# Kernel optimization log

Measured on AMD Instinct MI355X. Metric: run time of the kernel, lower is better.

Reference implementation:

```python
import jax, jax.numpy as jnp
import numpy as np

# ParamsJR('JR') defaults, all variances 0 -> fixed constants; w_bb and lm are the fit params.
DT = 1e-4                      # step_size
VMAX, V0, R = 5.0, 6.0, 0.56   # sigmoid params
U_UB = 500.0                   # u_2ndsys_ub
G_EFF = 0.01 + 1000.0          # lb + relu(g)
C1_EFF, C2_EFF = 0.01 + 135.0, 0.01 + 135.0 * 0.8
C3_EFF, C4_EFF = 0.01 + 135.0 * 0.25, 0.01 + 135.0 * 0.25
STD_EFF = 150.0 + 100.0        # noise_std_lb + relu(std_in)
K_EFF = 0.5 + 5.0              # k_lb + relu(k)
A_EFF, a_EFF = 3.25, 1.0 + 100.0   # 0+relu(A), 1+relu(a)
B_EFF, b_EFF = 22.0, 1.0 + 50.0    # 0+relu(B), 1+relu(b)
CY0, Y0, MU = 5.0, 2.0, 0.5
CONDUCT_LB = 1.5


def _sig(x):
    return VMAX / (1.0 + jnp.exp(R * (V0 - x)))


def _sys2nd(A, a, u, x, v):
    return A * a * u - 2.0 * a * v - a * a * x


def _sat(x):  # state saturation 1000*tanh(x/1000)
    return 1000.0 * jnp.tanh(x / 1000.0)


def setup_inputs() -> dict:
    N, H, B, OUT, BUF = 200, 20, 400, 64, 500
    key = jax.random.key(0)
    ks = jax.random.split(key, 7)
    return {
        "input": jax.random.normal(ks[0], (N, H, B), jnp.float32),
        "noise_in": jax.random.normal(ks[1], (N, H, B, 3), jnp.float32),
        "noise_out": jax.random.normal(ks[2], (N, B), jnp.float32),
        "hx": jax.random.uniform(ks[3], (N, 6), jnp.float32),
        "hE": jnp.zeros((N, BUF), jnp.float32),
        "w_bb": jnp.full((N, N), 0.05, jnp.float32),  # zeros + 0.05 init
        "lm": jax.random.normal(ks[4], (OUT, N), jnp.float32),
        "sc": jax.random.uniform(ks[5], (N, N), jnp.float32),
        "dist": jax.random.randint(ks[6], (N, N), 0, 100, dtype=jnp.int32),
    }


def _forward(input, noise_in, noise_out, hx, hE, w_bb, lm, sc, delays):
    OUT = lm.shape[0]
    # connectivity normalization (done once, outside the time loop, as in torch)
    w = jnp.exp(w_bb) * sc
    wl = jnp.log1p(0.5 * (w + w.T))
    w_n = wl / jnp.linalg.norm(wl)             # (N,N)
    dg = -jnp.diag(jnp.sum(w_n, axis=1))       # (N,N) Laplacian diagonal
    # lead-field normalization: rowwise L1 (torch: sqrt(lm**2).sum(1)), then column mean-center
    lm1 = lm / jnp.abs(lm).sum(axis=1, keepdims=True)
    lm_t = lm1 - lm1.sum(axis=0, keepdims=True) / OUT

    def inner(carry, xs):
        M, E, I, Mv, Ev, Iv, hEb = carry
        u, nE = xs                                              # (N,1) each
        Ed = jnp.take_along_axis(hEb, delays, axis=1)           # delayed M buffer
        LEd = jnp.sum(w_n * Ed.T, axis=1, keepdims=True)        # (N,1)
        rM = _sig(E - I)
        rE = STD_EFF * nE + G_EFF * (LEd + dg @ E) + C2_EFF * _sig(C1_EFF * M)
        rI = C4_EFF * _sig(C3_EFF * M)
        ddM = M + DT * Mv
        ddE = E + DT * Ev
        ddI = I + DT * Iv
        ddMv = Mv + DT * _sys2nd(A_EFF, a_EFF, U_UB * jnp.tanh(rM / U_UB), M, Mv)
        ddEv = Ev + DT * _sys2nd(A_EFF, a_EFF, K_EFF * u + U_UB * jnp.tanh(rE / U_UB), E, Ev)
        ddIv = Iv + DT * _sys2nd(B_EFF, b_EFF, U_UB * jnp.tanh(rI / U_UB), I, Iv)
        M, E, I = _sat(ddM), _sat(ddE), _sat(ddI)
        Mv, Ev, Iv = _sat(ddMv), _sat(ddEv), _sat(ddIv)
        hEb = hEb.at[:, 0].set(M[:, 0])
        return (M, E, I, Mv, Ev, Iv, hEb), None

    def outer(carry, xs):
        u_tr, n_tr = xs                                         # (H,N,1) each
        carry, _ = jax.lax.scan(inner, carry, (u_tr, n_tr))
        M, E, I, Mv, Ev, Iv, hEb = carry
        hEb = jnp.concatenate([M, hEb[:, :-1]], axis=1)         # shift delay buffer per TR
        eeg = CY0 * (lm_t @ (E - I)) - Y0                       # (OUT,1)
        return (M, E, I, Mv, Ev, Iv, hEb), eeg[:, 0]

    M, E, I = hx[:, 0:1], hx[:, 1:2], hx[:, 2:3]
    Mv, Ev, Iv = hx[:, 3:4], hx[:, 4:5], hx[:, 5:6]
    u_all = jnp.transpose(input, (2, 1, 0))[..., None]          # (B,H,N,1)
    nE_all = jnp.transpose(noise_in[..., 0], (2, 1, 0))[..., None]
    carry, eeg = jax.lax.scan(outer, (M, E, I, Mv, Ev, Iv, hE), (u_all, nE_all))
    M, E, I, Mv, Ev, Iv, _ = carry
    current_state = jnp.concatenate([M, E, I, Mv, Ev, Iv], axis=1)  # (N,6)
    return eeg.T, current_state                                 # eeg_batch (OUT,B)


def reference(input, noise_in, noise_out, hx, hE, w_bb, lm, sc, dist):
    delays = (dist.astype(jnp.float32) / (CONDUCT_LB + MU)).astype(jnp.int32)
    return _forward(input, noise_in, noise_out, hx, hE, w_bb, lm, sc, delays)
```

## Files before the change

kernel.cpp:

```cpp
#include <hip/hip_runtime.h>
#include <math.h>

namespace {

constexpr int N_   = 200;
constexpr int H_   = 20;
constexpr int B_   = 400;
constexpr int OUT_ = 64;
constexpr int BUF_ = 500;
constexpr int NT_  = 1024;
constexpr int HD_  = 50;
constexpr int HS_  = 51;
constexpr int GT0  = 224;
constexpr int NG_  = 800;
constexpr int EPT  = 50;
constexpr int CAP  = 16;
constexpr int UNR  = 12;

constexpr float L2E = 1.4426950408889634f;
constexpr float LN2 = 0.6931471805599453f;

constexpr float DT_  = 0.0001f;
constexpr float G_   = 1000.01f;
constexpr float C1_  = 135.01f;
constexpr float C2_  = 108.01f;
constexpr float C3_  = 33.76f;
constexpr float C4_  = 33.76f;
constexpr float STD_ = 250.0f;
constexpr float K_   = 5.5f;
constexpr float CY0_ = 5.0f;
constexpr float Y0_  = 2.0f;

constexpr float RL2E = 0.56f * L2E;
constexpr float V0R  = 6.0f * RL2E;
constexpr float TU_  = 2.0f * L2E / 500.0f;
constexpr float TS_  = 2.0f * L2E / 1000.0f;

constexpr float KMv = 0.9798f, KMu = 0.0328250f, KMx = 1.0201f;
constexpr float KEv = 0.9798f, KEu = 0.0328250f, KEx = 1.0201f;
constexpr float KIv = 0.9898f, KIu = 0.1122000f, KIx = 0.2601f;

__device__ __forceinline__ float fexp2(float x){ return __builtin_amdgcn_exp2f(x); }
__device__ __forceinline__ float flog2(float x){ return __builtin_amdgcn_logf(x); }
__device__ __forceinline__ float frcp (float x){ return __builtin_amdgcn_rcpf(x); }

__device__ __forceinline__ float sigf(float x){
    return 5.0f * frcp(1.0f + fexp2(fmaf(-RL2E, x, V0R)));
}
__device__ __forceinline__ float tanh500(float x){
    return 500.0f - 1000.0f * frcp(1.0f + fexp2(x * TU_));
}
__device__ __forceinline__ float satf(float x){
    return 1000.0f - 2000.0f * frcp(1.0f + fexp2(x * TS_));
}
__device__ __forceinline__ float wl_f(const float* __restrict__ wbb,
                                      const float* __restrict__ sc,
                                      int i, int j){
    float w0 = fexp2(wbb[i*N_+j]*L2E) * sc[i*N_+j];
    float w1 = fexp2(wbb[j*N_+i]*L2E) * sc[j*N_+i];
    return flog2(1.0f + 0.5f*(w0+w1)) * LN2;
}

__global__ void __launch_bounds__(NT_)
jansen_kernel(
    const float* __restrict__ input,
    const float* __restrict__ noise_in,
    const float* __restrict__ hx,
    const float* __restrict__ hEin,
    const float* __restrict__ wbb,
    const float* __restrict__ lm,
    const float* __restrict__ sc,
    const int*   __restrict__ dist,
    float* __restrict__ out,
    float2* __restrict__ tab)
{
    __shared__ float histT[N_*HS_];
    __shared__ float uslab[H_*N_];
    __shared__ float neslab[H_*N_];
    __shared__ float d0w_l[CAP*N_];
    __shared__ unsigned char d0j_l[CAP*N_];
    __shared__ float d1w_l[CAP*N_];
    __shared__ unsigned char d1j_l[CAP*N_];
    __shared__ float led_part[4*N_];
    __shared__ float mcol[2*N_];
    __shared__ float emi[N_];
    __shared__ float colmean[N_];
    __shared__ float lmrs[OUT_];
    __shared__ float red_s[NT_/64];
    __shared__ float norm_s;

    const int t = threadIdx.x;
    const bool isr = (t < N_);
    const bool isg = (t >= GT0);
    const int  gt  = t - GT0;
    const int  grow  = gt >> 2;
    const int  gslot = gt & 3;
    const int  jbase = gslot * EPT;
    const int  tb    = gt * EPT;

    int sidx[5];
    int goff[5];

    if (t < OUT_){
        float s2 = 0.f;
        for (int j=0;j<N_;++j) s2 += fabsf(lm[t*N_+j]);
        lmrs[t] = s2;
    }
    float M=0,E=0,I=0,Mv=0,Ev=0,Iv=0, rowsum=0, ledst=0;
    int cnt0=0, cnt1=0;
    #pragma unroll
    for (int r=0;r<5;++r){ sidx[r]=0; goff[r]=0; }
    if (isg){
        #pragma unroll
        for (int r=0;r<5;++r){
            int p = r*NG_ + gt;
            int hh = p / N_, ii = p - hh*N_;
            sidx[r] = hh*N_ + ii;
            goff[r] = ii*(H_*B_) + hh*B_;
            uslab[sidx[r]]  = input[goff[r]];
            neslab[sidx[r]] = noise_in[goff[r]*3];
        }
    }
    if (isr){
        for (int k=1;k<HD_;++k) histT[t*HS_ + (HD_-k)] = hEin[t*BUF_+k];
        mcol[t] = hEin[t*BUF_];
        M=hx[t*6+0]; E=hx[t*6+1]; I=hx[t*6+2];
        Mv=hx[t*6+3]; Ev=hx[t*6+4]; Iv=hx[t*6+5];
    }
    __syncthreads();

    float ss = 0.f, rs = 0.f;
    for (int m=0;m<EPT;++m){
        float w = 0.f; int d = 2;
        int j = jbase + m;
        if (isg){
            d = dist[j*N_+grow] >> 1;
            w = wl_f(wbb, sc, grow, j);
        }
        ss = fmaf(w,w,ss); rs += w;
        if (isg){
            int dm = (d<2) ? 2 : d;
            float ws = (d>=2) ? w : 0.f;
            tab[tb+m] = make_float2(ws, __uint_as_float((unsigned)j | ((unsigned)dm<<16)));
        }
    }
    if (isr){
        float cm=0.f;
        for (int o=0;o<OUT_;++o) cm += lm[o*N_+t] * frcp(lmrs[o]);
        colmean[t] = cm * (1.0f/(float)OUT_);
    }
    #pragma unroll
    for (int o=32;o>0;o>>=1) ss += __shfl_down(ss,o,64);
    if ((t&63)==0) red_s[t>>6] = ss;
    __syncthreads();
    if (t==0){ float tot=0.f; for (int w=0;w<NT_/64;++w) tot+=red_s[w]; norm_s = sqrtf(tot); }
    __syncthreads();
    const float inv = 1.0f / norm_s;
    if (isg){
        float* tf = (float*)tab;
        for (int m=0;m<EPT;++m) tf[2*(tb+m)] *= inv;
    }
    if (isg) led_part[gslot*N_+grow] = rs;

    float dw[UNR]; unsigned jpk[3];
    #pragma unroll
    for (int k=0;k<UNR;++k) dw[k] = 0.f;
    jpk[0]=jpk[1]=jpk[2]=0u;
    if (isr){
        #pragma unroll
        for (int k=0;k<UNR;++k){ d0w_l[k*N_+t]=0.f; d0j_l[k*N_+t]=0;
                                 d1w_l[k*N_+t]=0.f; d1j_l[k*N_+t]=0; }
        for (int j=0;j<N_;++j){
            int dd = dist[j*N_+t] >> 1;
            if (dd < 2){
                float w = wl_f(wbb, sc, t, j) * inv;
                if (dd==0){ if (cnt0<CAP){ d0w_l[cnt0*N_+t]=w; d0j_l[cnt0*N_+t]=(unsigned char)j; ++cnt0; } }
                else      { if (cnt1<CAP){ d1w_l[cnt1*N_+t]=w; d1j_l[cnt1*N_+t]=(unsigned char)j; ++cnt1; } }
            }
        }
        #pragma unroll
        for (int k=0;k<UNR;++k){
            dw[k] = d0w_l[k*N_+t];
            unsigned jv = d0j_l[k*N_+t];
            jpk[k>>2] |= jv << ((k&3)*8);
        }
    }
    __syncthreads();

    if (isr){
        rowsum = (led_part[t]+led_part[N_+t]+led_part[2*N_+t]+led_part[3*N_+t]) * inv;
    }
    __syncthreads();

    if (isg){
        float a0 = 0.f;
        for (int m=0;m<EPT;++m){
            float2 e = tab[tb+m];
            unsigned um = __float_as_uint(e.y);
            int c = HD_ - (int)(um>>16);
            a0 = fmaf(e.x, histT[(um&0xFFFFu)*HS_ + c], a0);
        }
        led_part[gslot*N_+grow] = a0;
    }
    __syncthreads();

    if (isr){
        float v = led_part[t]+led_part[N_+t]+led_part[2*N_+t]+led_part[3*N_+t];
        #pragma unroll
        for (int k=0;k<UNR;++k)
            v = fmaf(d1w_l[k*N_+t], histT[(int)d1j_l[k*N_+t]*HS_ + 49], v);
        for (int k=UNR;k<cnt1;++k)
            v = fmaf(d1w_l[k*N_+t], histT[(int)d1j_l[k*N_+t]*HS_ + 49], v);
        ledst = v;
    }
    __syncthreads();

#define ROW_BODY(MCR, MCW, HH)                                               \
    do {                                                                     \
        float rM  = sigf(E - I);                                             \
        float uM  = tanh500(rM);                                             \
        float Mn  = satf(fmaf(DT_, Mv, M));                                  \
        float Mvn = satf(fmaf(KMv, Mv, fmaf(KMu, uM, -KMx*M)));              \
        (MCW)[t] = Mn;                                                       \
        float rI  = C4_*sigf(C3_*M);                                         \
        float uI  = tanh500(rI);                                             \
        float In  = satf(fmaf(DT_, Iv, I));                                  \
        float Ivn = satf(fmaf(KIv, Iv, fmaf(KIu, uI, -KIx*I)));              \
        float u  = uslab[(HH)*N_+t];                                         \
        float ne = neslab[(HH)*N_+t];                                        \
        float l0 = ledst, l1 = 0.f, l2 = 0.f, l3 = 0.f;                      \
        _Pragma("unroll")                                                    \
        for (int k=0;k<UNR;++k){                                             \
            int j = (jpk[k>>2] >> ((k&3)*8)) & 255;                          \
            float v = (MCR)[j];                                              \
            if      ((k&3)==0) l0 = fmaf(dw[k], v, l0);                      \
            else if ((k&3)==1) l1 = fmaf(dw[k], v, l1);                      \
            else if ((k&3)==2) l2 = fmaf(dw[k], v, l2);                      \
            else               l3 = fmaf(dw[k], v, l3);                      \
        }                                                                    \
        for (int k=UNR;k<cnt0;++k)                                           \
            l0 = fmaf(d0w_l[k*N_+t], (MCR)[d0j_l[k*N_+t]], l0);              \
        float LEd = (l0+l1)+(l2+l3);                                         \
        float rE  = fmaf(STD_, ne, G_*(LEd - rowsum*E)) + C2_*sigf(C1_*M);   \
        float uE  = fmaf(K_, u, tanh500(rE));                                \
        float En  = satf(fmaf(DT_, Ev, E));                                  \
        float Evn = satf(fmaf(KEv, Ev, fmaf(KEu, uE, -KEx*E)));              \
        M=Mn; Mv=Mvn; I=In; Iv=Ivn; E=En; Ev=Evn;                            \
    } while(0)

#define GUSE(W, Mt)                                                         \
    do {                                                                     \
        unsigned um = __float_as_uint(Mt);                                   \
        int c = ts - (int)(um>>16); if (c<0) c += HD_;                       \
        acc = fmaf((W), histT[(um&0xFFFFu)*HS_ + c], acc);                   \
    } while(0)

    float pw0=0,pm0=0,pw1=0,pm1=0;
    float tw0=0,tm0=0,tw1=0,tm1=0,tw2=0,tm2=0;
    if (isg){
        float2 e0 = tab[tb+0]; pw0=e0.x; pm0=e0.y;
        float2 e1 = tab[tb+1]; pw1=e1.x; pm1=e1.y;
    }

    int smod = 0;
    for (int s=0; s<B_; ++s){
        int ts = smod+1; if (ts==HD_) ts = 0;
        float acc = 0.f;
        for (int q=0; q<10; ++q){
            if (isg){
                GUSE(pw0, pm0);
                GUSE(pw1, pm1);
                float2 e;
                e = tab[tb + 5*q + 2]; tw0=e.x; tm0=e.y;
                e = tab[tb + 5*q + 3]; tw1=e.x; tm1=e.y;
                e = tab[tb + 5*q + 4]; tw2=e.x; tm2=e.y;
            }
            if (isr) ROW_BODY(mcol, mcol+N_, 2*q);
            __syncthreads();
            if (isg){
                GUSE(tw0, tm0);
                GUSE(tw1, tm1);
                GUSE(tw2, tm2);
                int nb = (q==9) ? 0 : 5*(q+1);
                float2 e;
                e = tab[tb + nb];     pw0=e.x; pm0=e.y;
                e = tab[tb + nb + 1]; pw1=e.x; pm1=e.y;
            }
            if (isr) ROW_BODY(mcol+N_, mcol, 2*q+1);
            __syncthreads();
        }
        if (isr){ histT[t*HS_ + smod] = M; emi[t] = E - I; }
        if (isg){
            led_part[gslot*N_+grow] = acc;
            int sn = s+1; if (sn >= B_) sn = B_-1;
            #pragma unroll
            for (int r=0;r<5;++r){
                uslab[sidx[r]]  = input[goff[r] + sn];
                neslab[sidx[r]] = noise_in[(goff[r] + sn)*3];
            }
        }
        __syncthreads();
        if (isr){
            float v = led_part[t]+led_part[N_+t]+led_part[2*N_+t]+led_part[3*N_+t];
            #pragma unroll
            for (int k=0;k<UNR;++k)
                v = fmaf(d1w_l[k*N_+t], mcol[d1j_l[k*N_+t]], v);
            for (int k=UNR;k<cnt1;++k)
                v = fmaf(d1w_l[k*N_+t], mcol[d1j_l[k*N_+t]], v);
            ledst = v;
        }
        {
            int o = t>>4, l = t&15;
            float il = frcp(lmrs[o]);
            float a2 = 0.f;
            for (int j=l;j<N_;j+=16)
                a2 = fmaf(fmaf(lm[o*N_+j], il, -colmean[j]), emi[j], a2);
            a2 += __shfl_down(a2,8,16); a2 += __shfl_down(a2,4,16);
            a2 += __shfl_down(a2,2,16); a2 += __shfl_down(a2,1,16);
            if (l==0) out[o*B_+s] = fmaf(CY0_, a2, -Y0_);
        }
        smod = ts;
        __syncthreads();
    }

#undef ROW_BODY
#undef GUSE

    if (isr){
        float* cs = out + OUT_*B_ + t*6;
        cs[0]=M; cs[1]=E; cs[2]=I; cs[3]=Mv; cs[4]=Ev; cs[5]=Iv;
    }
}

}

extern "C" void kernel_launch(void* const* d_in, const int* in_sizes, int n_in,
                              void* d_out, int out_size, void* d_ws, size_t ws_size,
                              hipStream_t stream)
{
    const float* input    = (const float*)d_in[0];
    const float* noise_in = (const float*)d_in[1];
    const float* hx   = (const float*)d_in[3];
    const float* hEin = (const float*)d_in[4];
    const float* wbb  = (const float*)d_in[5];
    const float* lm   = (const float*)d_in[6];
    const float* sc   = (const float*)d_in[7];
    const int*   dist = (const int*)d_in[8];
    float* out = (float*)d_out;
    float2* tab = (float2*)((char*)d_ws + 1024);

    hipLaunchKernelGGL(jansen_kernel, dim3(1), dim3(NT_), 0, stream,
                       input, noise_in, hx, hEin, wbb, lm, sc, dist, out, tab);
}
```

Baseline: 6.598 ms.

## Process four inner steps per barrier using lookahead M predictions

Restructures the inner integration so each block barrier covers four time steps instead of one. Because M depends only on E and I with a lag, future M values (M1..M3) can be computed ahead and published as a float4 per node, letting the delayed-coupling sums for four steps be gathered at once. This cuts the 20 barriers per TR down to 5. It also switches the input/noise slabs to a node-major float4 layout and vectorises the delay-table reads. The price is a longer, register-heavier row body and careful carry of the state across the skewed pipeline.

```diff
diff --git a/kernel.cpp b/kernel.cpp
--- a/kernel.cpp
+++ b/kernel.cpp
@@ -75,19 +75,22 @@
     float2* __restrict__ tab)
 {
     __shared__ float histT[N_*HS_];
-    __shared__ float uslab[H_*N_];
-    __shared__ float neslab[H_*N_];
+    __shared__ float4 uslab4[N_*(H_/4)];
+    __shared__ float4 neslab4[N_*(H_/4)];
     __shared__ float d0w_l[CAP*N_];
     __shared__ unsigned char d0j_l[CAP*N_];
     __shared__ float d1w_l[CAP*N_];
     __shared__ unsigned char d1j_l[CAP*N_];
     __shared__ float led_part[4*N_];
-    __shared__ float mcol[2*N_];
+    __shared__ float4 mcol4[2*N_];
     __shared__ float emi[N_];
     __shared__ float colmean[N_];
     __shared__ float lmrs[OUT_];
     __shared__ float red_s[NT_/64];
     __shared__ float norm_s;
+
+    float* uslabF  = (float*)uslab4;
+    float* neslabF = (float*)neslab4;
 
     const int t = threadIdx.x;
     const bool isr = (t < N_);
@@ -115,15 +118,14 @@
         for (int r=0;r<5;++r){
             int p = r*NG_ + gt;
             int hh = p / N_, ii = p - hh*N_;
-            sidx[r] = hh*N_ + ii;
+            sidx[r] = ii*H_ + hh;
             goff[r] = ii*(H_*B_) + hh*B_;
-            uslab[sidx[r]]  = input[goff[r]];
-            neslab[sidx[r]] = noise_in[goff[r]*3];
+            uslabF[sidx[r]]  = input[goff[r]];
+            neslabF[sidx[r]] = noise_in[goff[r]*3];
         }
     }
     if (isr){
         for (int k=1;k<HD_;++k) histT[t*HS_ + (HD_-k)] = hEin[t*BUF_+k];
-        mcol[t] = hEin[t*BUF_];
         M=hx[t*6+0]; E=hx[t*6+1]; I=hx[t*6+2];
         Mv=hx[t*6+3]; Ev=hx[t*6+4]; Iv=hx[t*6+5];
     }
@@ -213,100 +215,144 @@
             v = fmaf(d1w_l[k*N_+t], histT[(int)d1j_l[k*N_+t]*HS_ + 49], v);
         ledst = v;
     }
-    __syncthreads();
-
-#define ROW_BODY(MCR, MCW, HH)                                               \
-    do {                                                                     \
-        float rM  = sigf(E - I);                                             \
-        float uM  = tanh500(rM);                                             \
-        float Mn  = satf(fmaf(DT_, Mv, M));                                  \
-        float Mvn = satf(fmaf(KMv, Mv, fmaf(KMu, uM, -KMx*M)));              \
-        (MCW)[t] = Mn;                                                       \
-        float rI  = C4_*sigf(C3_*M);                                         \
-        float uI  = tanh500(rI);                                             \
-        float In  = satf(fmaf(DT_, Iv, I));                                  \
-        float Ivn = satf(fmaf(KIv, Iv, fmaf(KIu, uI, -KIx*I)));              \
-        float u  = uslab[(HH)*N_+t];                                         \
-        float ne = neslab[(HH)*N_+t];                                        \
-        float l0 = ledst, l1 = 0.f, l2 = 0.f, l3 = 0.f;                      \
-        _Pragma("unroll")                                                    \
-        for (int k=0;k<UNR;++k){                                             \
-            int j = (jpk[k>>2] >> ((k&3)*8)) & 255;                          \
-            float v = (MCR)[j];                                              \
-            if      ((k&3)==0) l0 = fmaf(dw[k], v, l0);                      \
-            else if ((k&3)==1) l1 = fmaf(dw[k], v, l1);                      \
-            else if ((k&3)==2) l2 = fmaf(dw[k], v, l2);                      \
-            else               l3 = fmaf(dw[k], v, l3);                      \
-        }                                                                    \
-        for (int k=UNR;k<cnt0;++k)                                           \
-            l0 = fmaf(d0w_l[k*N_+t], (MCR)[d0j_l[k*N_+t]], l0);              \
-        float LEd = (l0+l1)+(l2+l3);                                         \
-        float rE  = fmaf(STD_, ne, G_*(LEd - rowsum*E)) + C2_*sigf(C1_*M);   \
-        float uE  = fmaf(K_, u, tanh500(rE));                                \
-        float En  = satf(fmaf(DT_, Ev, E));                                  \
-        float Evn = satf(fmaf(KEv, Ev, fmaf(KEu, uE, -KEx*E)));              \
-        M=Mn; Mv=Mvn; I=In; Iv=Ivn; E=En; Ev=Evn;                            \
-    } while(0)
-
-#define GUSE(W, Mt)                                                         \
-    do {                                                                     \
-        unsigned um = __float_as_uint(Mt);                                   \
-        int c = ts - (int)(um>>16); if (c<0) c += HD_;                       \
-        acc = fmaf((W), histT[(um&0xFFFFu)*HS_ + c], acc);                   \
-    } while(0)
-
-    float pw0=0,pm0=0,pw1=0,pm1=0;
-    float tw0=0,tm0=0,tw1=0,tm1=0,tw2=0,tm2=0;
-    if (isg){
-        float2 e0 = tab[tb+0]; pw0=e0.x; pm0=e0.y;
-        float2 e1 = tab[tb+1]; pw1=e1.x; pm1=e1.y;
-    }
+
+    float E0=E, E1=0, Ev0=Ev, I0=I, I1=0, Iv0=Iv;
+    float Mv2=0, M0=M, M1=0, M2=0, M3=0, MvOut=Mv;
+    if (isr){
+        E1 = satf(fmaf(DT_, Ev0, E0));
+        I1 = satf(fmaf(DT_, Iv0, I0));
+        float uM0 = tanh500(sigf(E0 - I0));
+        float Mv1 = satf(fmaf(KMv, Mv, fmaf(KMu, uM0, -KMx*M0)));
+        M1 = satf(fmaf(DT_, Mv, M0));
+        float uM1 = tanh500(sigf(E1 - I1));
+        Mv2 = satf(fmaf(KMv, Mv1, fmaf(KMu, uM1, -KMx*M1)));
+        M2 = satf(fmaf(DT_, Mv1, M1));
+        M3 = satf(fmaf(DT_, Mv2, M2));
+        mcol4[t] = make_float4(hEin[t*BUF_], M1, M2, M3);
+    }
+    __syncthreads();
 
     int smod = 0;
+    int P = 0;
     for (int s=0; s<B_; ++s){
         int ts = smod+1; if (ts==HD_) ts = 0;
         float acc = 0.f;
-        for (int q=0; q<10; ++q){
+        #pragma unroll 1
+        for (int q=0; q<5; ++q){
             if (isg){
-                GUSE(pw0, pm0);
-                GUSE(pw1, pm1);
-                float2 e;
-                e = tab[tb + 5*q + 2]; tw0=e.x; tm0=e.y;
-                e = tab[tb + 5*q + 3]; tw1=e.x; tm1=e.y;
-                e = tab[tb + 5*q + 4]; tw2=e.x; tm2=e.y;
+                const float4* t4 = (const float4*)(tab + tb + q*10);
+                #pragma unroll
+                for (int m=0;m<5;++m){
+                    float4 ee = t4[m];
+                    unsigned um0 = __float_as_uint(ee.y);
+                    int c0 = ts - (int)(um0>>16); if (c0<0) c0 += HD_;
+                    acc = fmaf(ee.x, histT[(um0&0xFFFFu)*HS_ + c0], acc);
+                    unsigned um1 = __float_as_uint(ee.w);
+                    int c1 = ts - (int)(um1>>16); if (c1<0) c1 += HD_;
+                    acc = fmaf(ee.z, histT[(um1&0xFFFFu)*HS_ + c1], acc);
+                }
             }
-            if (isr) ROW_BODY(mcol, mcol+N_, 2*q);
+            if (isr){
+                const float4* rb = mcol4 + (P&1)*N_;
+                float4*       wb = mcol4 + ((P+1)&1)*N_;
+                float p00=ledst, p01=0.f, p02=0.f, p03=0.f;
+                float p10=ledst, p11=0.f, p12=0.f, p13=0.f;
+                float p20=ledst, p21=0.f, p22=0.f, p23=0.f;
+                float p30=ledst, p31=0.f, p32=0.f, p33=0.f;
+                #pragma unroll
+                for (int k=0;k<UNR;++k){
+                    int j = (jpk[k>>2] >> ((k&3)*8)) & 255;
+                    float4 mj = rb[j];
+                    float w = dw[k];
+                    if ((k&3)==0){ p00=fmaf(w,mj.x,p00); p10=fmaf(w,mj.y,p10);
+                                   p20=fmaf(w,mj.z,p20); p30=fmaf(w,mj.w,p30); }
+                    else if ((k&3)==1){ p01=fmaf(w,mj.x,p01); p11=fmaf(w,mj.y,p11);
+                                        p21=fmaf(w,mj.z,p21); p31=fmaf(w,mj.w,p31); }
+                    else if ((k&3)==2){ p02=fmaf(w,mj.x,p02); p12=fmaf(w,mj.y,p12);
+                                        p22=fmaf(w,mj.z,p22); p32=fmaf(w,mj.w,p32); }
+                    else              { p03=fmaf(w,mj.x,p03); p13=fmaf(w,mj.y,p13);
+                                        p23=fmaf(w,mj.z,p23); p33=fmaf(w,mj.w,p33); }
+                }
+                for (int k=UNR;k<cnt0;++k){
+                    float w = d0w_l[k*N_+t];
+                    float4 mj = rb[d0j_l[k*N_+t]];
+                    p00=fmaf(w,mj.x,p00); p10=fmaf(w,mj.y,p10);
+                    p20=fmaf(w,mj.z,p20); p30=fmaf(w,mj.w,p30);
+                }
+                float la0 = (p00+p01)+(p02+p03);
+                float la1 = (p10+p11)+(p12+p13);
+                float la2 = (p20+p21)+(p22+p23);
+                float la3 = (p30+p31)+(p32+p33);
+                const float4 uu = uslab4[t*(H_/4)+q];
+                const float4 nn = neslab4[t*(H_/4)+q];
+                float rE0 = fmaf(STD_, nn.x, G_*(la0 - rowsum*E0)) + C2_*sigf(C1_*M0);
+                float uE0 = fmaf(K_, uu.x, tanh500(rE0));
+                float Ev1 = satf(fmaf(KEv, Ev0, fmaf(KEu, uE0, -KEx*E0)));
+                float E2  = satf(fmaf(DT_, Ev1, E1));
+                float uI0 = tanh500(C4_*sigf(C3_*M0));
+                float Iv1 = satf(fmaf(KIv, Iv0, fmaf(KIu, uI0, -KIx*I0)));
+                float I2  = satf(fmaf(DT_, Iv1, I1));
+                float uM2 = tanh500(sigf(E2 - I2));
+                float Mv3 = satf(fmaf(KMv, Mv2, fmaf(KMu, uM2, -KMx*M2)));
+                float M4  = satf(fmaf(DT_, Mv3, M3));
+                float rE1 = fmaf(STD_, nn.y, G_*(la1 - rowsum*E1)) + C2_*sigf(C1_*M1);
+                float uE1 = fmaf(K_, uu.y, tanh500(rE1));
+                float Ev2 = satf(fmaf(KEv, Ev1, fmaf(KEu, uE1, -KEx*E1)));
+                float E3  = satf(fmaf(DT_, Ev2, E2));
+                float uI1 = tanh500(C4_*sigf(C3_*M1));
+                float Iv2 = satf(fmaf(KIv, Iv1, fmaf(KIu, uI1, -KIx*I1)));
+                float I3  = satf(fmaf(DT_, Iv2, I2));
+                float uM3 = tanh500(sigf(E3 - I3));
+                float Mv4 = satf(fmaf(KMv, Mv3, fmaf(KMu, uM3, -KMx*M3)));
+                float M5  = satf(fmaf(DT_, Mv4, M4));
+                float rE2 = fmaf(STD_, nn.z, G_*(la2 - rowsum*E2)) + C2_*sigf(C1_*M2);
+                float uE2 = fmaf(K_, uu.z, tanh500(rE2));
+                float Ev3 = satf(fmaf(KEv, Ev2, fmaf(KEu, uE2, -KEx*E2)));
+                float E4  = satf(fmaf(DT_, Ev3, E3));
+                float uI2 = tanh500(C4_*sigf(C3_*M2));
+                float Iv3 = satf(fmaf(KIv, Iv2, fmaf(KIu, uI2, -KIx*I2)));
+                float I4  = satf(fmaf(DT_, Iv3, I3));
+                float uM4 = tanh500(sigf(E4 - I4));
+                float Mv5 = satf(fmaf(KMv, Mv4, fmaf(KMu, uM4, -KMx*M4)));
+                float M6  = satf(fmaf(DT_, Mv5, M5));
+                float rE3 = fmaf(STD_, nn.w, G_*(la3 - rowsum*E3)) + C2_*sigf(C1_*M3);
+                float uE3 = fmaf(K_, uu.w, tanh500(rE3));
+                float Ev4 = satf(fmaf(KEv, Ev3, fmaf(KEu, uE3, -KEx*E3)));
+                float E5  = satf(fmaf(DT_, Ev4, E4));
+                float uI3 = tanh500(C4_*sigf(C3_*M3));
+                float Iv4 = satf(fmaf(KIv, Iv3, fmaf(KIu, uI3, -KIx*I3)));
+                float I5  = satf(fmaf(DT_, Iv4, I4));
+                float uM5 = tanh500(sigf(E5 - I5));
+                float Mv6 = satf(fmaf(KMv, Mv5, fmaf(KMu, uM5, -KMx*M5)));
+                float M7  = satf(fmaf(DT_, Mv6, M6));
+                wb[t] = make_float4(M4, M5, M6, M7);
+                MvOut = Mv4;
+                E0=E4; E1=E5; Ev0=Ev4;
+                I0=I4; I1=I5; Iv0=Iv4;
+                Mv2=Mv6; M0=M4; M1=M5; M2=M6; M3=M7;
+            }
+            ++P;
             __syncthreads();
-            if (isg){
-                GUSE(tw0, tm0);
-                GUSE(tw1, tm1);
-                GUSE(tw2, tm2);
-                int nb = (q==9) ? 0 : 5*(q+1);
-                float2 e;
-                e = tab[tb + nb];     pw0=e.x; pm0=e.y;
-                e = tab[tb + nb + 1]; pw1=e.x; pm1=e.y;
-            }
-            if (isr) ROW_BODY(mcol+N_, mcol, 2*q+1);
-            __syncthreads();
-        }
-        if (isr){ histT[t*HS_ + smod] = M; emi[t] = E - I; }
+        }
+        if (isr){ histT[t*HS_ + smod] = M0; emi[t] = E0 - I0; }
         if (isg){
             led_part[gslot*N_+grow] = acc;
             int sn = s+1; if (sn >= B_) sn = B_-1;
             #pragma unroll
             for (int r=0;r<5;++r){
-                uslab[sidx[r]]  = input[goff[r] + sn];
-                neslab[sidx[r]] = noise_in[(goff[r] + sn)*3];
+                uslabF[sidx[r]]  = input[goff[r] + sn];
+                neslabF[sidx[r]] = noise_in[(goff[r] + sn)*3];
             }
         }
         __syncthreads();
         if (isr){
+            const float4* rb2 = mcol4 + (P&1)*N_;
             float v = led_part[t]+led_part[N_+t]+led_part[2*N_+t]+led_part[3*N_+t];
             #pragma unroll
             for (int k=0;k<UNR;++k)
-                v = fmaf(d1w_l[k*N_+t], mcol[d1j_l[k*N_+t]], v);
+                v = fmaf(d1w_l[k*N_+t], rb2[d1j_l[k*N_+t]].x, v);
             for (int k=UNR;k<cnt1;++k)
-                v = fmaf(d1w_l[k*N_+t], mcol[d1j_l[k*N_+t]], v);
+                v = fmaf(d1w_l[k*N_+t], rb2[d1j_l[k*N_+t]].x, v);
             ledst = v;
         }
         {
@@ -323,12 +369,9 @@
         __syncthreads();
     }
 
-#undef ROW_BODY
-#undef GUSE
-
     if (isr){
         float* cs = out + OUT_*B_ + t*6;
-        cs[0]=M; cs[1]=E; cs[2]=I; cs[3]=Mv; cs[4]=Ev; cs[5]=Iv;
+        cs[0]=M0; cs[1]=E0; cs[2]=I0; cs[3]=MvOut; cs[4]=Ev0; cs[5]=Iv0;
     }
 }
 
```

After: 7.491 ms. 1.14x slower.

## Split row waves from gather waves with custom LDS barrier among row waves

Applied to the files above, without the earlier changes.

The first 256 threads (4 waves) now run the 20 inner recurrence steps per TR and synchronise among themselves with an LDS atomic counter and spin-wait barrier, replacing the block-wide __syncthreads. The remaining 768 threads do the delayed-history gather for the next TR in one pass using float4 table loads, then prefetch the next slab of input and noise into registers. They write that slab to LDS only after the block barrier. The aim is to cut the per-substep barrier cost across all 16 waves. The trade-off is spin-wait polling and reliance on wave-level memory ordering for correctness.

```diff
diff --git a/kernel.cpp b/kernel.cpp
--- a/kernel.cpp
+++ b/kernel.cpp
@@ -16,6 +16,9 @@
 constexpr int EPT  = 50;
 constexpr int CAP  = 16;
 constexpr int UNR  = 12;
+constexpr int RW_  = 256;
+constexpr int NFREE = NT_ - RW_;
+constexpr int SLAB  = H_ * N_;
 
 constexpr float L2E = 1.4426950408889634f;
 constexpr float LN2 = 0.6931471805599453f;
@@ -88,6 +91,7 @@
     __shared__ float lmrs[OUT_];
     __shared__ float red_s[NT_/64];
     __shared__ float norm_s;
+    __shared__ int   rbar;
 
     const int t = threadIdx.x;
     const bool isr = (t < N_);
@@ -101,6 +105,7 @@
     int sidx[5];
     int goff[5];
 
+    if (t == 0) rbar = 0;
     if (t < OUT_){
         float s2 = 0.f;
         for (int j=0;j<N_;++j) s2 += fabsf(lm[t*N_+j]);
@@ -212,6 +217,22 @@
         for (int k=UNR;k<cnt1;++k)
             v = fmaf(d1w_l[k*N_+t], histT[(int)d1j_l[k*N_+t]*HS_ + 49], v);
         ledst = v;
+    }
+
+    const int gf = t - RW_;
+    int sidxM[6], goffM[6];
+    bool has6 = false;
+    if (t >= RW_){
+        #pragma unroll
+        for (int r=0;r<6;++r){
+            int p = r*NFREE + gf;
+            if (p < SLAB){
+                int hh = p / N_, ii = p - hh*N_;
+                sidxM[r] = hh*N_ + ii;
+                goffM[r] = ii*(H_*B_) + hh*B_;
+            } else { sidxM[r]=0; goffM[r]=0; }
+        }
+        has6 = (5*NFREE + gf) < SLAB;
     }
     __syncthreads();
 
@@ -248,55 +269,71 @@
         M=Mn; Mv=Mvn; I=In; Iv=Ivn; E=En; Ev=Evn;                            \
     } while(0)
 
-#define GUSE(W, Mt)                                                         \
+#define ROW_SYNC()                                                           \
     do {                                                                     \
-        unsigned um = __float_as_uint(Mt);                                   \
-        int c = ts - (int)(um>>16); if (c<0) c += HD_;                       \
-        acc = fmaf((W), histT[(um&0xFFFFu)*HS_ + c], acc);                   \
+        asm volatile("s_waitcnt lgkmcnt(0)" ::: "memory");                   \
+        if ((t & 63) == 0) atomicAdd(&rbar, 1);                              \
+        ++repoch;                                                            \
+        while (*(volatile int*)&rbar < 4*repoch)                             \
+            __builtin_amdgcn_s_sleep(1);                                     \
+        asm volatile("" ::: "memory");                                       \
     } while(0)
 
-    float pw0=0,pm0=0,pw1=0,pm1=0;
-    float tw0=0,tm0=0,tw1=0,tm1=0,tw2=0,tm2=0;
-    if (isg){
-        float2 e0 = tab[tb+0]; pw0=e0.x; pm0=e0.y;
-        float2 e1 = tab[tb+1]; pw1=e1.x; pm1=e1.y;
-    }
-
     int smod = 0;
+    int repoch = 0;
+    float su_r[6], sn_r[6];
     for (int s=0; s<B_; ++s){
         int ts = smod+1; if (ts==HD_) ts = 0;
-        float acc = 0.f;
-        for (int q=0; q<10; ++q){
-            if (isg){
-                GUSE(pw0, pm0);
-                GUSE(pw1, pm1);
-                float2 e;
-                e = tab[tb + 5*q + 2]; tw0=e.x; tm0=e.y;
-                e = tab[tb + 5*q + 3]; tw1=e.x; tm1=e.y;
-                e = tab[tb + 5*q + 4]; tw2=e.x; tm2=e.y;
-            }
-            if (isr) ROW_BODY(mcol, mcol+N_, 2*q);
-            __syncthreads();
-            if (isg){
-                GUSE(tw0, tm0);
-                GUSE(tw1, tm1);
-                GUSE(tw2, tm2);
-                int nb = (q==9) ? 0 : 5*(q+1);
-                float2 e;
-                e = tab[tb + nb];     pw0=e.x; pm0=e.y;
-                e = tab[tb + nb + 1]; pw1=e.x; pm1=e.y;
-            }
-            if (isr) ROW_BODY(mcol+N_, mcol, 2*q+1);
-            __syncthreads();
-        }
-        if (isr){ histT[t*HS_ + smod] = M; emi[t] = E - I; }
-        if (isg){
-            led_part[gslot*N_+grow] = acc;
+        if (t < RW_){
+            int cur = 0;
+            #pragma unroll 2
+            for (int h=0; h<H_; ++h){
+                if (isr) ROW_BODY(mcol + cur*N_, mcol + (cur^1)*N_, h);
+                ROW_SYNC();
+                cur ^= 1;
+            }
+            if (isr){ histT[t*HS_ + smod] = M; emi[t] = E - I; }
+        } else {
+            float acc = 0.f;
+            {
+                const float4* t4 = (const float4*)(tab + (size_t)gf*EPT);
+                #pragma unroll 5
+                for (int m=0;m<EPT/2;++m){
+                    float4 ee = t4[m];
+                    unsigned um0 = __float_as_uint(ee.y);
+                    int c0 = ts - (int)(um0>>16); if (c0<0) c0 += HD_;
+                    acc = fmaf(ee.x, histT[(um0&0xFFFFu)*HS_ + c0], acc);
+                    unsigned um1 = __float_as_uint(ee.w);
+                    int c1 = ts - (int)(um1>>16); if (c1<0) c1 += HD_;
+                    acc = fmaf(ee.z, histT[(um1&0xFFFFu)*HS_ + c1], acc);
+                }
+            }
+            led_part[(gf&3)*N_ + (gf>>2)] = acc;
+            if (gf < NG_-NFREE){
+                const int u1 = NFREE + gf;
+                float acc1 = 0.f;
+                const float4* t4 = (const float4*)(tab + (size_t)u1*EPT);
+                #pragma unroll 5
+                for (int m=0;m<EPT/2;++m){
+                    float4 ee = t4[m];
+                    unsigned um0 = __float_as_uint(ee.y);
+                    int c0 = ts - (int)(um0>>16); if (c0<0) c0 += HD_;
+                    acc1 = fmaf(ee.x, histT[(um0&0xFFFFu)*HS_ + c0], acc1);
+                    unsigned um1 = __float_as_uint(ee.w);
+                    int c1 = ts - (int)(um1>>16); if (c1<0) c1 += HD_;
+                    acc1 = fmaf(ee.z, histT[(um1&0xFFFFu)*HS_ + c1], acc1);
+                }
+                led_part[(u1&3)*N_ + (u1>>2)] = acc1;
+            }
             int sn = s+1; if (sn >= B_) sn = B_-1;
             #pragma unroll
             for (int r=0;r<5;++r){
-                uslab[sidx[r]]  = input[goff[r] + sn];
-                neslab[sidx[r]] = noise_in[(goff[r] + sn)*3];
+                su_r[r] = input[goffM[r] + sn];
+                sn_r[r] = noise_in[(goffM[r] + sn)*3];
+            }
+            if (has6){
+                su_r[5] = input[goffM[5] + sn];
+                sn_r[5] = noise_in[(goffM[5] + sn)*3];
             }
         }
         __syncthreads();
@@ -309,6 +346,14 @@
                 v = fmaf(d1w_l[k*N_+t], mcol[d1j_l[k*N_+t]], v);
             ledst = v;
         }
+        if (t >= RW_){
+            #pragma unroll
+            for (int r=0;r<5;++r){
+                uslab[sidxM[r]]  = su_r[r];
+                neslab[sidxM[r]] = sn_r[r];
+            }
+            if (has6){ uslab[sidxM[5]] = su_r[5]; neslab[sidxM[5]] = sn_r[5]; }
+        }
         {
             int o = t>>4, l = t&15;
             float il = frcp(lmrs[o]);
@@ -324,7 +369,7 @@
     }
 
 #undef ROW_BODY
-#undef GUSE
+#undef ROW_SYNC
 
     if (isr){
         float* cs = out + OUT_*B_ + t*6;
```

New measurement: 5.937 ms. 10.0% less time.
